# Kernel tuning notes

Measured on AMD Instinct MI355X. Metric: run time of the kernel, lower is better.

Reference implementation:

```python
import jax, jax.numpy as jnp
import numpy as np

M_LEN = 1024
BATCH = 16384


def setup_inputs() -> dict:
    key = jax.random.key(0)
    k0, k1, k2, k3, kw = jax.random.split(key, 5)
    mod0 = jax.random.normal(k0, (BATCH, M_LEN), dtype=jnp.float32)
    mod1 = jax.random.normal(k1, (BATCH, M_LEN), dtype=jnp.float32)
    mod2 = jax.random.normal(k2, (BATCH, M_LEN), dtype=jnp.float32)
    mod3 = jax.random.normal(k3, (BATCH, M_LEN), dtype=jnp.float32)
    # simulate missing modality for first quarter of patients (exercises rescale path)
    mod1 = mod1.at[: BATCH // 4].set(0.0)
    W = jax.random.normal(kw, (M_LEN, M_LEN), dtype=jnp.float32) * (1.0 / np.sqrt(M_LEN))
    return {"mod0": mod0, "mod1": mod1, "mod2": mod2, "mod3": mod3, "W": W}


def reference(mod0, mod1, mod2, mod3, W):
    ndata = jnp.stack([mod0, mod1, mod2, mod3])          # [M, B, L]
    scores = jnp.einsum("mbl,kl->mbk", ndata, W)          # Linear (no bias): x @ W.T
    attention_weights = jax.nn.softmax(scores, axis=0)    # softmax over modalities
    fused = jnp.sum(ndata * attention_weights, axis=0)    # [B, L]
    # vectorized replacement of per-patient python loop:
    # count modalities whose sum is exactly zero; if >0, scale row by (count+1)
    zero_dims = jnp.sum(jnp.sum(ndata, axis=2) == 0.0, axis=0)          # [B] int
    scaler = jnp.where(zero_dims > 0, zero_dims + 1, 1).astype(fused.dtype)
    return fused * scaler[:, None]
```

## Files before the change

### kernel.cpp

```cpp
#include <hip/hip_runtime.h>
#include <hip/hip_bf16.h>

#define M_LEN 1024
#define BATCH 16384

#define BM 128
#define BN 128
#define BK 64
#define THREADS 256

typedef __attribute__((ext_vector_type(8))) short bf16x8;
typedef __attribute__((ext_vector_type(4))) float f32x4;
typedef unsigned short ushort_t;


__device__ __forceinline__ ushort_t bf16_rne(float f) {
    unsigned u = __float_as_uint(f);
    unsigned r = u + 0x7FFFu + ((u >> 16) & 1u);
    return (ushort_t)(r >> 16);
}

__device__ __forceinline__ float bf16_to_f(ushort_t u) {
    return __uint_as_float(((unsigned)u) << 16);
}

__device__ __forceinline__ unsigned pack2(float lo, float hi) {
    return __builtin_amdgcn_perm(__float_as_uint(hi), __float_as_uint(lo), 0x07060302u);
}

__device__ __forceinline__ void gload_lds16(const void* g, void* l) {
    __builtin_amdgcn_global_load_lds(
        (const __attribute__((address_space(1))) unsigned int*)g,
        (__attribute__((address_space(3))) unsigned int*)l,
        16, 0, 0);
}

__device__ __forceinline__ float4 ntload4(const float4* p) {
    f32x4 v = __builtin_nontemporal_load((const f32x4*)p);
    return make_float4(v.x, v.y, v.z, v.w);
}

__global__ __launch_bounds__(THREADS) void convert_pass(
    const float* __restrict__ mod0, const float* __restrict__ mod1,
    const float* __restrict__ mod2, const float* __restrict__ mod3,
    const float* __restrict__ W,
    ushort_t* __restrict__ Ab, ushort_t* __restrict__ Wb, int* __restrict__ zf)
{
    const int blk  = blockIdx.x;
    const int wave = threadIdx.x >> 6;
    const int lane = threadIdx.x & 63;

    if (blk < BATCH) {
        const int b = blk, m = wave;
        const float* mp = (m == 0) ? mod0 : (m == 1) ? mod1 : (m == 2) ? mod2 : mod3;
        const float4* row = (const float4*)(mp + (size_t)b * M_LEN);
        ushort_t* dst = Ab + ((size_t)b * 4 + m) * M_LEN;
        unsigned orr = 0u;
        #pragma unroll
        for (int j = 0; j < 4; ++j) {
            float4 v = ntload4(&row[j * 64 + lane]);
            orr |= (__float_as_uint(v.x) | __float_as_uint(v.y) |
                    __float_as_uint(v.z) | __float_as_uint(v.w)) << 1;
            ushort4 o;
            o.x = bf16_rne(v.x); o.y = bf16_rne(v.y);
            o.z = bf16_rne(v.z); o.w = bf16_rne(v.w);
            ((ushort4*)dst)[j * 64 + lane] = o;
        }
        const int nz = __any(orr != 0u);
        if (lane == 0) zf[b * 4 + m] = nz ? 0 : 1;
    } else {
        const int r = (blk - BATCH) * 4 + wave;
        const float4* row = (const float4*)(W + (size_t)r * M_LEN);
        ushort_t* dst = Wb + (size_t)r * M_LEN;
        #pragma unroll
        for (int j = 0; j < 4; ++j) {
            float4 v = row[j * 64 + lane];
            ushort4 o;
            o.x = bf16_rne(v.x); o.y = bf16_rne(v.y);
            o.z = bf16_rne(v.z); o.w = bf16_rne(v.w);
            ((ushort4*)dst)[j * 64 + lane] = o;
        }
    }
}

__global__ __launch_bounds__(THREADS) void gemm_fused(
    const ushort_t* __restrict__ Ab, const ushort_t* __restrict__ Wb,
    const int* __restrict__ zf, float* __restrict__ out)
{
    __shared__ __align__(16) ushort_t As[BM * BK];
    __shared__ __align__(16) ushort_t Bs[BN * BK];
    __shared__ float scalerS[BM / 4];

    const int t    = threadIdx.x;
    const int lane = t & 63;
    const int wave = t >> 6;
    const int quad = lane >> 4;
    const int ln15 = lane & 15;
    const int wm   = wave >> 1;
    const int wn   = wave & 1;

    const int colb = blockIdx.x;
    const int rowb = blockIdx.y;
    const int row0 = rowb * BM;
    const int col0 = colb * BN;

    if (t < 32) {
        const int4 f = ((const int4*)zf)[rowb * 32 + t];
        const int z = f.x + f.y + f.z + f.w;
        scalerS[t] = (z > 0) ? (float)(z + 1) : 1.0f;
    }

    const int rloc = (lane >> 3);
    const int c    = (lane & 7) ^ rloc;
    const ushort_t* aPtr[4];
    const ushort_t* bPtr[4];
    #pragma unroll
    for (int q = 0; q < 4; ++q) {
        const int r = wave * 32 + q * 8 + rloc;
        aPtr[q] = Ab + (size_t)(row0 + r) * M_LEN + c * 8;
        bPtr[q] = Wb + (size_t)(col0 + r) * M_LEN + c * 8;
    }

    f32x4 acc[4][4];
    #pragma unroll
    for (int i = 0; i < 4; ++i)
        #pragma unroll
        for (int j = 0; j < 4; ++j)
            acc[i][j] = (f32x4){0.f, 0.f, 0.f, 0.f};

    const unsigned slotB   = (unsigned)(quad ^ (ln15 & 7));
    const unsigned aRowOff = (unsigned)((wm * 64 + ln15) * 64);
    const unsigned bRowOff = (unsigned)((wn * 64 + ln15) * 64);

    for (int kt = 0; kt < 16; ++kt) {
        #pragma unroll
        for (int q = 0; q < 4; ++q) {
            gload_lds16(aPtr[q], &As[(wave * 4 + q) * 512]);
            gload_lds16(bPtr[q], &Bs[(wave * 4 + q) * 512]);
            aPtr[q] += BK;
            bPtr[q] += BK;
        }
        __syncthreads();
        #pragma unroll
        for (int ks = 0; ks < 2; ++ks) {
            const unsigned slot8 = (slotB ^ (unsigned)(ks * 4)) * 8u;
            bf16x8 af[4], bfr[4];
            #pragma unroll
            for (int i = 0; i < 4; ++i)
                af[i] = *(const bf16x8*)(&As[aRowOff + i * 1024 + slot8]);
            #pragma unroll
            for (int j = 0; j < 4; ++j)
                bfr[j] = *(const bf16x8*)(&Bs[bRowOff + j * 1024 + slot8]);
            #pragma unroll
            for (int i = 0; i < 4; ++i)
                #pragma unroll
                for (int j = 0; j < 4; ++j)
                    acc[i][j] = __builtin_amdgcn_mfma_f32_16x16x32_bf16(
                        af[i], bfr[j], acc[i][j], 0, 0, 0);
        }
        __syncthreads();
    }

    #pragma unroll
    for (int i = 0; i < 4; ++i) {
        const int bl = wm * 16 + i * 4 + quad;
        const int b  = rowb * 32 + bl;
        const float scal = scalerS[bl];
        const ushort_t* xr = Ab + (size_t)b * 4 * M_LEN;
        #pragma unroll
        for (int j = 0; j < 4; ++j) {
            const int k = col0 + wn * 64 + j * 16 + ln15;
            const float x0 = bf16_to_f(xr[k]);
            const float x1 = bf16_to_f(xr[M_LEN + k]);
            const float x2 = bf16_to_f(xr[2 * M_LEN + k]);
            const float x3 = bf16_to_f(xr[3 * M_LEN + k]);
            const f32x4 s = acc[i][j];
            const float mx = fmaxf(fmaxf(s.x, s.y), fmaxf(s.z, s.w));
            const float e0 = __expf(s.x - mx);
            const float e1 = __expf(s.y - mx);
            const float e2 = __expf(s.z - mx);
            const float e3 = __expf(s.w - mx);
            const float num = e0 * x0 + e1 * x1 + e2 * x2 + e3 * x3;
            const float v = num * scal / (e0 + e1 + e2 + e3);
            __builtin_nontemporal_store(v, &out[(size_t)b * M_LEN + k]);
        }
    }
}

__global__ __launch_bounds__(THREADS) void fused_modal_attn(
    const float* __restrict__ mod0, const float* __restrict__ mod1,
    const float* __restrict__ mod2, const float* __restrict__ mod3,
    const float* __restrict__ W, float* __restrict__ out)
{
    __shared__ __align__(16) unsigned short As[BM * BK];
    __shared__ __align__(16) unsigned short Bs[BN * BK];
    __shared__ unsigned rowOr[BM];
    __shared__ float scalerS[BM / 4];

    const int t    = threadIdx.x;
    const int lane = t & 63;
    const int wave = t >> 6;
    const int quad = lane >> 4;
    const int ln15 = lane & 15;
    const int wm   = wave >> 1;
    const int wn   = wave & 1;

    const int colb = blockIdx.x;
    const int rowb = blockIdx.y;
    const int row0 = rowb * BM;
    const int col0 = colb * BN;

    if (t < BM) rowOr[t] = 0u;

    const int sr  = t >> 3;
    const int scl = t & 7;

    const float* ap[4];
    const float* bp[4];
    unsigned ldsOff[4];
    unsigned orAcc[4] = {0u, 0u, 0u, 0u};
    #pragma unroll
    for (int j = 0; j < 4; ++j) {
        const int r  = j * 32 + sr;
        const int gr = row0 + r;
        const int b  = gr >> 2;
        const int m  = gr & 3;
        const float* mp = (m == 0) ? mod0 : (m == 1) ? mod1 : (m == 2) ? mod2 : mod3;
        ap[j] = mp + (size_t)b * M_LEN + scl * 8;
        bp[j] = W + (size_t)(col0 + r) * M_LEN + scl * 8;
        ldsOff[j] = (unsigned)(r * 64 + ((scl ^ (r & 7)) * 8));
    }

    f32x4 acc[4][4];
    #pragma unroll
    for (int i = 0; i < 4; ++i)
        #pragma unroll
        for (int j = 0; j < 4; ++j)
            acc[i][j] = (f32x4){0.f, 0.f, 0.f, 0.f};

    const unsigned slotB   = (unsigned)(quad ^ (ln15 & 7));
    const unsigned aRowOff = (unsigned)((wm * 64 + ln15) * 64);
    const unsigned bRowOff = (unsigned)((wn * 64 + ln15) * 64);

    for (int it = 0; it < 16; ++it) {
        __syncthreads();
        #pragma unroll
        for (int j = 0; j < 4; ++j) {
            const float4* pa = (const float4*)ap[j];
            const float4* pb = (const float4*)bp[j];
            float4 a0 = pa[0], a1 = pa[1];
            float4 b0 = pb[0], b1 = pb[1];
            ap[j] += BK; bp[j] += BK;

            unsigned pA0 = pack2(a0.x, a0.y), pA1 = pack2(a0.z, a0.w);
            unsigned pA2 = pack2(a1.x, a1.y), pA3 = pack2(a1.z, a1.w);
            orAcc[j] |= (pA0 | pA1) | (pA2 | pA3);
            *(uint4*)(&As[ldsOff[j]]) = make_uint4(pA0, pA1, pA2, pA3);

            unsigned pB0 = pack2(b0.x, b0.y), pB1 = pack2(b0.z, b0.w);
            unsigned pB2 = pack2(b1.x, b1.y), pB3 = pack2(b1.z, b1.w);
            *(uint4*)(&Bs[ldsOff[j]]) = make_uint4(pB0, pB1, pB2, pB3);
        }
        __syncthreads();
        #pragma unroll
        for (int ks = 0; ks < 2; ++ks) {
            const unsigned slot8 = (slotB ^ (unsigned)(ks * 4)) * 8u;
            bf16x8 af[4], bfr[4];
            #pragma unroll
            for (int i = 0; i < 4; ++i)
                af[i] = *(const bf16x8*)(&As[aRowOff + i * 1024 + slot8]);
            #pragma unroll
            for (int j = 0; j < 4; ++j)
                bfr[j] = *(const bf16x8*)(&Bs[bRowOff + j * 1024 + slot8]);
            #pragma unroll
            for (int i = 0; i < 4; ++i)
                #pragma unroll
                for (int j = 0; j < 4; ++j)
                    acc[i][j] = __builtin_amdgcn_mfma_f32_16x16x32_bf16(
                        af[i], bfr[j], acc[i][j], 0, 0, 0);
        }
    }

    #pragma unroll
    for (int j = 0; j < 4; ++j)
        atomicOr(&rowOr[j * 32 + sr], orAcc[j]);
    __syncthreads();
    if (t < 32) {
        const int z = (rowOr[4 * t + 0] == 0u) + (rowOr[4 * t + 1] == 0u)
                    + (rowOr[4 * t + 2] == 0u) + (rowOr[4 * t + 3] == 0u);
        scalerS[t] = (z > 0) ? (float)(z + 1) : 1.0f;
    }
    __syncthreads();

    #pragma unroll
    for (int i = 0; i < 4; ++i) {
        const int bl = wm * 16 + i * 4 + quad;
        const int b  = rowb * 32 + bl;
        const float scal = scalerS[bl];
        #pragma unroll
        for (int j = 0; j < 4; ++j) {
            const int k = col0 + wn * 64 + j * 16 + ln15;
            const size_t off = (size_t)b * M_LEN + k;
            const float x0 = mod0[off], x1 = mod1[off];
            const float x2 = mod2[off], x3 = mod3[off];
            const f32x4 s = acc[i][j];
            const float mx = fmaxf(fmaxf(s.x, s.y), fmaxf(s.z, s.w));
            const float e0 = __expf(s.x - mx);
            const float e1 = __expf(s.y - mx);
            const float e2 = __expf(s.z - mx);
            const float e3 = __expf(s.w - mx);
            const float num = e0 * x0 + e1 * x1 + e2 * x2 + e3 * x3;
            out[off] = num * scal / (e0 + e1 + e2 + e3);
        }
    }
}

extern "C" void kernel_launch(void* const* d_in, const int* in_sizes, int n_in,
                              void* d_out, int out_size, void* d_ws, size_t ws_size,
                              hipStream_t stream) {
    const float* mod0 = (const float*)d_in[0];
    const float* mod1 = (const float*)d_in[1];
    const float* mod2 = (const float*)d_in[2];
    const float* mod3 = (const float*)d_in[3];
    const float* W    = (const float*)d_in[4];
    float* out = (float*)d_out;

    const size_t abBytes = (size_t)4 * BATCH * M_LEN * sizeof(ushort_t);
    const size_t wbBytes = (size_t)M_LEN * M_LEN * sizeof(ushort_t);
    const size_t zfBytes = (size_t)4 * BATCH * sizeof(int);
    const size_t need = abBytes + wbBytes + zfBytes;

    if (ws_size >= need) {
        ushort_t* Ab = (ushort_t*)d_ws;
        ushort_t* Wb = (ushort_t*)((char*)d_ws + abBytes);
        int*      zfp = (int*)((char*)d_ws + abBytes + wbBytes);

        convert_pass<<<dim3(BATCH + M_LEN / 4), dim3(THREADS), 0, stream>>>(
            mod0, mod1, mod2, mod3, W, Ab, Wb, zfp);

        dim3 grid(M_LEN / BN, (4 * BATCH) / BM);
        gemm_fused<<<grid, dim3(THREADS), 0, stream>>>(Ab, Wb, zfp, out);
    } else {
        dim3 grid(M_LEN / BN, (4 * BATCH) / BM);
        fused_modal_attn<<<grid, dim3(THREADS), 0, stream>>>(
            mod0, mod1, mod2, mod3, W, out);
    }
}
```

Measured before the change: 410.8 us.

## Double-buffer GEMM with async LDS loads, larger tiles and swizzled block order

```diff
diff --git a/kernel.cpp b/kernel.cpp
--- a/kernel.cpp
+++ b/kernel.cpp
@@ -8,6 +8,11 @@
 #define BN 128
 #define BK 64
 #define THREADS 256
+
+#define BM3 256
+#define BN3 128
+#define BK3 32
+#define GTHREADS 512
 
 typedef __attribute__((ext_vector_type(8))) short bf16x8;
 typedef __attribute__((ext_vector_type(4))) float f32x4;
@@ -83,13 +88,15 @@
     }
 }
 
-__global__ __launch_bounds__(THREADS) void gemm_fused(
+__global__ __launch_bounds__(GTHREADS, 4) void gemm_tlp(
     const ushort_t* __restrict__ Ab, const ushort_t* __restrict__ Wb,
     const int* __restrict__ zf, float* __restrict__ out)
 {
-    __shared__ __align__(16) ushort_t As[BM * BK];
-    __shared__ __align__(16) ushort_t Bs[BN * BK];
-    __shared__ float scalerS[BM / 4];
+    __shared__ __align__(16) ushort_t As0[BM3 * BK3];
+    __shared__ __align__(16) ushort_t As1[BM3 * BK3];
+    __shared__ __align__(16) ushort_t Bs0[BN3 * BK3];
+    __shared__ __align__(16) ushort_t Bs1[BN3 * BK3];
+    __shared__ float scalerS[BM3 / 4];
 
     const int t    = threadIdx.x;
     const int lane = t & 63;
@@ -99,26 +106,165 @@
     const int wm   = wave >> 1;
     const int wn   = wave & 1;
 
+    const int bid  = blockIdx.x;
+    const int wid  = (bid & 7) * 256 + (bid >> 3);
+    const int colb = wid & 7;
+    const int rowb = wid >> 3;
+    const int row0 = rowb * BM3;
+    const int col0 = colb * BN3;
+
+    if (t < 64) {
+        const int4 f = ((const int4*)zf)[rowb * 64 + t];
+        const int z = f.x + f.y + f.z + f.w;
+        scalerS[t] = (z > 0) ? (float)(z + 1) : 1.0f;
+    }
+
+    const int rl = lane >> 2;
+    const int c4 = (lane & 3) ^ (rl & 3);
+    const ushort_t* aP[2];
+    const ushort_t* bP;
+    unsigned aD[2], bD;
+    #pragma unroll
+    for (int r = 0; r < 2; ++r) {
+        const int arow = r * 128 + wave * 16 + rl;
+        aP[r] = Ab + (size_t)(row0 + arow) * M_LEN + c4 * 8;
+        aD[r] = (unsigned)((r * 128 + wave * 16) * BK3);
+    }
+    {
+        const int brow = wave * 16 + rl;
+        bP = Wb + (size_t)(col0 + brow) * M_LEN + c4 * 8;
+        bD = (unsigned)((wave * 16) * BK3);
+    }
+
+    #define STAGE(AD_, BD_)                                             \
+        do {                                                            \
+            gload_lds16(aP[0], (AD_) + aD[0]); aP[0] += BK3;            \
+            gload_lds16(aP[1], (AD_) + aD[1]); aP[1] += BK3;            \
+            gload_lds16(bP,    (BD_) + bD);    bP    += BK3;            \
+        } while (0)
+
+    f32x4 acc[4][4];
+    #pragma unroll
+    for (int i = 0; i < 4; ++i)
+        #pragma unroll
+        for (int j = 0; j < 4; ++j)
+            acc[i][j] = (f32x4){0.f, 0.f, 0.f, 0.f};
+
+    const unsigned slotOff = (unsigned)((quad ^ (ln15 & 3)) * 8);
+    const unsigned aOff = (unsigned)((wm * 64 + ln15) * BK3) + slotOff;
+    const unsigned bOff = (unsigned)((wn * 64 + ln15) * BK3) + slotOff;
+
+    auto compute = [&](const ushort_t* As_, const ushort_t* Bs_) {
+        bf16x8 af[4], bfr[4];
+        #pragma unroll
+        for (int j = 0; j < 4; ++j)
+            bfr[j] = *(const bf16x8*)(&Bs_[bOff + j * 16 * BK3]);
+        #pragma unroll
+        for (int i = 0; i < 4; ++i)
+            af[i] = *(const bf16x8*)(&As_[aOff + i * 16 * BK3]);
+        __builtin_amdgcn_s_setprio(1);
+        #pragma unroll
+        for (int i = 0; i < 4; ++i)
+            #pragma unroll
+            for (int j = 0; j < 4; ++j)
+                acc[i][j] = __builtin_amdgcn_mfma_f32_16x16x32_bf16(
+                    af[i], bfr[j], acc[i][j], 0, 0, 0);
+        __builtin_amdgcn_s_setprio(0);
+    };
+
+    STAGE(As0, Bs0);
+    STAGE(As1, Bs1);
+    asm volatile("s_waitcnt vmcnt(3) lgkmcnt(0)" ::: "memory");
+    __builtin_amdgcn_s_barrier();
+
+    #pragma unroll 1
+    for (int t2 = 0; t2 < 15; ++t2) {
+        compute(As0, Bs0);
+        __builtin_amdgcn_s_barrier();
+        STAGE(As0, Bs0);
+        asm volatile("s_waitcnt vmcnt(3)" ::: "memory");
+        __builtin_amdgcn_s_barrier();
+
+        compute(As1, Bs1);
+        __builtin_amdgcn_s_barrier();
+        STAGE(As1, Bs1);
+        asm volatile("s_waitcnt vmcnt(3)" ::: "memory");
+        __builtin_amdgcn_s_barrier();
+    }
+    compute(As0, Bs0);
+    asm volatile("s_waitcnt vmcnt(0)" ::: "memory");
+    __builtin_amdgcn_s_barrier();
+    compute(As1, Bs1);
+
+    #pragma unroll
+    for (int i = 0; i < 4; ++i) {
+        const int bl = wm * 16 + i * 4 + quad;
+        const int b  = rowb * 64 + bl;
+        const float scal = scalerS[bl];
+        const ushort_t* xr = Ab + (size_t)b * 4 * M_LEN;
+        #pragma unroll
+        for (int j = 0; j < 4; ++j) {
+            const int k = col0 + wn * 64 + j * 16 + ln15;
+            const float x0 = bf16_to_f(xr[k]);
+            const float x1 = bf16_to_f(xr[M_LEN + k]);
+            const float x2 = bf16_to_f(xr[2 * M_LEN + k]);
+            const float x3 = bf16_to_f(xr[3 * M_LEN + k]);
+            const f32x4 s = acc[i][j];
+            const float mx = fmaxf(fmaxf(s.x, s.y), fmaxf(s.z, s.w));
+            const float e0 = __expf(s.x - mx);
+            const float e1 = __expf(s.y - mx);
+            const float e2 = __expf(s.z - mx);
+            const float e3 = __expf(s.w - mx);
+            const float num = e0 * x0 + e1 * x1 + e2 * x2 + e3 * x3;
+            const float v = num * scal / (e0 + e1 + e2 + e3);
+            __builtin_nontemporal_store(v, &out[(size_t)b * M_LEN + k]);
+        }
+    }
+    #undef STAGE
+}
+
+__global__ __launch_bounds__(THREADS) void fused_modal_attn(
+    const float* __restrict__ mod0, const float* __restrict__ mod1,
+    const float* __restrict__ mod2, const float* __restrict__ mod3,
+    const float* __restrict__ W, float* __restrict__ out)
+{
+    __shared__ __align__(16) unsigned short As[BM * BK];
+    __shared__ __align__(16) unsigned short Bs[BN * BK];
+    __shared__ unsigned rowOr[BM];
+    __shared__ float scalerS[BM / 4];
+
+    const int t    = threadIdx.x;
+    const int lane = t & 63;
+    const int wave = t >> 6;
+    const int quad = lane >> 4;
+    const int ln15 = lane & 15;
+    const int wm   = wave >> 1;
+    const int wn   = wave & 1;
+
     const int colb = blockIdx.x;
     const int rowb = blockIdx.y;
     const int row0 = rowb * BM;
     const int col0 = colb * BN;
 
-    if (t < 32) {
-        const int4 f = ((const int4*)zf)[rowb * 32 + t];
-        const int z = f.x + f.y + f.z + f.w;
-        scalerS[t] = (z > 0) ? (float)(z + 1) : 1.0f;
-    }
-
-    const int rloc = (lane >> 3);
-    const int c    = (lane & 7) ^ rloc;
-    const ushort_t* aPtr[4];
-    const ushort_t* bPtr[4];
-    #pragma unroll
-    for (int q = 0; q < 4; ++q) {
-        const int r = wave * 32 + q * 8 + rloc;
-        aPtr[q] = Ab + (size_t)(row0 + r) * M_LEN + c * 8;
-        bPtr[q] = Wb + (size_t)(col0 + r) * M_LEN + c * 8;
+    if (t < BM) rowOr[t] = 0u;
+
+    const int sr  = t >> 3;
+    const int scl = t & 7;
+
+    const float* ap[4];
+    const float* bp[4];
+    unsigned ldsOff[4];
+    unsigned orAcc[4] = {0u, 0u, 0u, 0u};
+    #pragma unroll
+    for (int j = 0; j < 4; ++j) {
+        const int r  = j * 32 + sr;
+        const int gr = row0 + r;
+        const int b  = gr >> 2;
+        const int m  = gr & 3;
+        const float* mp = (m == 0) ? mod0 : (m == 1) ? mod1 : (m == 2) ? mod2 : mod3;
+        ap[j] = mp + (size_t)b * M_LEN + scl * 8;
+        bp[j] = W + (size_t)(col0 + r) * M_LEN + scl * 8;
+        ldsOff[j] = (unsigned)(r * 64 + ((scl ^ (r & 7)) * 8));
     }
 
     f32x4 acc[4][4];
@@ -132,13 +278,24 @@
     const unsigned aRowOff = (unsigned)((wm * 64 + ln15) * 64);
     const unsigned bRowOff = (unsigned)((wn * 64 + ln15) * 64);
 
-    for (int kt = 0; kt < 16; ++kt) {
-        #pragma unroll
-        for (int q = 0; q < 4; ++q) {
-            gload_lds16(aPtr[q], &As[(wave * 4 + q) * 512]);
-            gload_lds16(bPtr[q], &Bs[(wave * 4 + q) * 512]);
-            aPtr[q] += BK;
-            bPtr[q] += BK;
+    for (int it = 0; it < 16; ++it) {
+        __syncthreads();
+        #pragma unroll
+        for (int j = 0; j < 4; ++j) {
+            const float4* pa = (const float4*)ap[j];
+            const float4* pb = (const float4*)bp[j];
+            float4 a0 = pa[0], a1 = pa[1];
+            float4 b0 = pb[0], b1 = pb[1];
+            ap[j] += BK; bp[j] += BK;
+
+            unsigned pA0 = pack2(a0.x, a0.y), pA1 = pack2(a0.z, a0.w);
+            unsigned pA2 = pack2(a1.x, a1.y), pA3 = pack2(a1.z, a1.w);
+            orAcc[j] |= (pA0 | pA1) | (pA2 | pA3);
+            *(uint4*)(&As[ldsOff[j]]) = make_uint4(pA0, pA1, pA2, pA3);
+
+            unsigned pB0 = pack2(b0.x, b0.y), pB1 = pack2(b0.z, b0.w);
+            unsigned pB2 = pack2(b1.x, b1.y), pB3 = pack2(b1.z, b1.w);
+            *(uint4*)(&Bs[ldsOff[j]]) = make_uint4(pB0, pB1, pB2, pB3);
         }
         __syncthreads();
         #pragma unroll
@@ -158,127 +315,6 @@
                     acc[i][j] = __builtin_amdgcn_mfma_f32_16x16x32_bf16(
                         af[i], bfr[j], acc[i][j], 0, 0, 0);
         }
-        __syncthreads();
-    }
-
-    #pragma unroll
-    for (int i = 0; i < 4; ++i) {
-        const int bl = wm * 16 + i * 4 + quad;
-        const int b  = rowb * 32 + bl;
-        const float scal = scalerS[bl];
-        const ushort_t* xr = Ab + (size_t)b * 4 * M_LEN;
-        #pragma unroll
-        for (int j = 0; j < 4; ++j) {
-            const int k = col0 + wn * 64 + j * 16 + ln15;
-            const float x0 = bf16_to_f(xr[k]);
-            const float x1 = bf16_to_f(xr[M_LEN + k]);
-            const float x2 = bf16_to_f(xr[2 * M_LEN + k]);
-            const float x3 = bf16_to_f(xr[3 * M_LEN + k]);
-            const f32x4 s = acc[i][j];
-            const float mx = fmaxf(fmaxf(s.x, s.y), fmaxf(s.z, s.w));
-            const float e0 = __expf(s.x - mx);
-            const float e1 = __expf(s.y - mx);
-            const float e2 = __expf(s.z - mx);
-            const float e3 = __expf(s.w - mx);
-            const float num = e0 * x0 + e1 * x1 + e2 * x2 + e3 * x3;
-            const float v = num * scal / (e0 + e1 + e2 + e3);
-            __builtin_nontemporal_store(v, &out[(size_t)b * M_LEN + k]);
-        }
-    }
-}
-
-__global__ __launch_bounds__(THREADS) void fused_modal_attn(
-    const float* __restrict__ mod0, const float* __restrict__ mod1,
-    const float* __restrict__ mod2, const float* __restrict__ mod3,
-    const float* __restrict__ W, float* __restrict__ out)
-{
-    __shared__ __align__(16) unsigned short As[BM * BK];
-    __shared__ __align__(16) unsigned short Bs[BN * BK];
-    __shared__ unsigned rowOr[BM];
-    __shared__ float scalerS[BM / 4];
-
-    const int t    = threadIdx.x;
-    const int lane = t & 63;
-    const int wave = t >> 6;
-    const int quad = lane >> 4;
-    const int ln15 = lane & 15;
-    const int wm   = wave >> 1;
-    const int wn   = wave & 1;
-
-    const int colb = blockIdx.x;
-    const int rowb = blockIdx.y;
-    const int row0 = rowb * BM;
-    const int col0 = colb * BN;
-
-    if (t < BM) rowOr[t] = 0u;
-
-    const int sr  = t >> 3;
-    const int scl = t & 7;
-
-    const float* ap[4];
-    const float* bp[4];
-    unsigned ldsOff[4];
-    unsigned orAcc[4] = {0u, 0u, 0u, 0u};
-    #pragma unroll
-    for (int j = 0; j < 4; ++j) {
-        const int r  = j * 32 + sr;
-        const int gr = row0 + r;
-        const int b  = gr >> 2;
-        const int m  = gr & 3;
-        const float* mp = (m == 0) ? mod0 : (m == 1) ? mod1 : (m == 2) ? mod2 : mod3;
-        ap[j] = mp + (size_t)b * M_LEN + scl * 8;
-        bp[j] = W + (size_t)(col0 + r) * M_LEN + scl * 8;
-        ldsOff[j] = (unsigned)(r * 64 + ((scl ^ (r & 7)) * 8));
-    }
-
-    f32x4 acc[4][4];
-    #pragma unroll
-    for (int i = 0; i < 4; ++i)
-        #pragma unroll
-        for (int j = 0; j < 4; ++j)
-            acc[i][j] = (f32x4){0.f, 0.f, 0.f, 0.f};
-
-    const unsigned slotB   = (unsigned)(quad ^ (ln15 & 7));
-    const unsigned aRowOff = (unsigned)((wm * 64 + ln15) * 64);
-    const unsigned bRowOff = (unsigned)((wn * 64 + ln15) * 64);
-
-    for (int it = 0; it < 16; ++it) {
-        __syncthreads();
-        #pragma unroll
-        for (int j = 0; j < 4; ++j) {
-            const float4* pa = (const float4*)ap[j];
-            const float4* pb = (const float4*)bp[j];
-            float4 a0 = pa[0], a1 = pa[1];
-            float4 b0 = pb[0], b1 = pb[1];
-            ap[j] += BK; bp[j] += BK;
-
-            unsigned pA0 = pack2(a0.x, a0.y), pA1 = pack2(a0.z, a0.w);
-            unsigned pA2 = pack2(a1.x, a1.y), pA3 = pack2(a1.z, a1.w);
-            orAcc[j] |= (pA0 | pA1) | (pA2 | pA3);
-            *(uint4*)(&As[ldsOff[j]]) = make_uint4(pA0, pA1, pA2, pA3);
-
-            unsigned pB0 = pack2(b0.x, b0.y), pB1 = pack2(b0.z, b0.w);
-            unsigned pB2 = pack2(b1.x, b1.y), pB3 = pack2(b1.z, b1.w);
-            *(uint4*)(&Bs[ldsOff[j]]) = make_uint4(pB0, pB1, pB2, pB3);
-        }
-        __syncthreads();
-        #pragma unroll
-        for (int ks = 0; ks < 2; ++ks) {
-            const unsigned slot8 = (slotB ^ (unsigned)(ks * 4)) * 8u;
-            bf16x8 af[4], bfr[4];
-            #pragma unroll
-            for (int i = 0; i < 4; ++i)
-                af[i] = *(const bf16x8*)(&As[aRowOff + i * 1024 + slot8]);
-            #pragma unroll
-            for (int j = 0; j < 4; ++j)
-                bfr[j] = *(const bf16x8*)(&Bs[bRowOff + j * 1024 + slot8]);
-            #pragma unroll
-            for (int i = 0; i < 4; ++i)
-                #pragma unroll
-                for (int j = 0; j < 4; ++j)
-                    acc[i][j] = __builtin_amdgcn_mfma_f32_16x16x32_bf16(
-                        af[i], bfr[j], acc[i][j], 0, 0, 0);
-        }
     }
 
     #pragma unroll
@@ -338,8 +374,8 @@
         convert_pass<<<dim3(BATCH + M_LEN / 4), dim3(THREADS), 0, stream>>>(
             mod0, mod1, mod2, mod3, W, Ab, Wb, zfp);
 
-        dim3 grid(M_LEN / BN, (4 * BATCH) / BM);
-        gemm_fused<<<grid, dim3(THREADS), 0, stream>>>(Ab, Wb, zfp, out);
+        gemm_tlp<<<dim3((M_LEN / BN3) * ((4 * BATCH) / BM3)), dim3(GTHREADS), 0, stream>>>(
+            Ab, Wb, zfp, out);
     } else {
         dim3 grid(M_LEN / BN, (4 * BATCH) / BM);
         fused_modal_attn<<<grid, dim3(THREADS), 0, stream>>>(
```

Result: faster. 386.8 us (-5.8%).
